# Optimization experiments

Measured on AMD Instinct MI355X. Metric: run time of the kernel, lower is better.

The kernel has to match this reference:

```python
import jax, jax.numpy as jnp
import numpy as np

N = 131072
F_IN = 256
FEATURES = 64
N_SOURCES = 32


def setup_inputs() -> dict:
    key = jax.random.key(0)
    k1, k2, k3 = jax.random.split(key, 3)
    x = jax.random.normal(k1, (N, F_IN), dtype=jnp.float32)
    source = jax.random.randint(k2, (N,), 0, N_SOURCES, dtype=jnp.int32)
    W = jax.random.normal(k3, (F_IN, N_SOURCES * FEATURES), dtype=jnp.float32) * (1.0 / np.sqrt(F_IN))
    b = jnp.zeros((N_SOURCES * FEATURES,), dtype=jnp.float32)
    return {"x": x, "source": source, "W": W, "b": b}


def reference(x, source, W, b):
    # Dense projection to all sources: (N, n_sources*features)
    y = jnp.dot(x, W) + b
    # Per-row gather of the slice belonging to this row's source id.
    # Equivalent to y[i, source[i]*FEATURES : (source[i]+1)*FEATURES].
    y = y.reshape(x.shape[0], N_SOURCES, FEATURES)
    out = jnp.take_along_axis(y, source[:, None, None].astype(jnp.int32), axis=1)
    return out[:, 0, :]  # (N, FEATURES)
```

## Files before the change

kernel.cpp:

```cpp
#include <hip/hip_runtime.h>

#define N_ROWS   131072
#define F_IN     256
#define FEAT     64
#define NSRC     32
#define WSTRIDE  (NSRC * FEAT)
#define NCH      32
#define CHUNK    4096
#define NCB      (N_ROWS / 256)
#define CBPC     16
#define CAPC     44
#define SEG      (CAPC + 1)
#define LCAP     320
#define TR       16
#define TPAD     66

#define MCHUNK   4096
#define LCAP1    512
#define KPAD     264

typedef __attribute__((ext_vector_type(8))) short  bf16x8;
typedef __attribute__((ext_vector_type(4))) float  f32x4;

#define WAITV(N)  asm volatile("s_waitcnt vmcnt(" #N ")" ::: "memory")
#define WAITLGKM() asm volatile("s_waitcnt lgkmcnt(0)" ::: "memory")
#define SBAR()    do { __builtin_amdgcn_s_barrier(); __builtin_amdgcn_sched_barrier(0); } while (0)

__device__ __forceinline__ unsigned short f2bf(float f) {
    union { float f; unsigned u; } c; c.f = f;
    unsigned r = c.u + 0x7fffu + ((c.u >> 16) & 1u);
    return (unsigned short)(r >> 16);
}

__device__ __forceinline__ bf16x8 pack8(f32x4 f0, f32x4 f1) {
    bf16x8 a;
    a[0] = (short)f2bf(f0[0]); a[1] = (short)f2bf(f0[1]);
    a[2] = (short)f2bf(f0[2]); a[3] = (short)f2bf(f0[3]);
    a[4] = (short)f2bf(f1[0]); a[5] = (short)f2bf(f1[1]);
    a[6] = (short)f2bf(f1[2]); a[7] = (short)f2bf(f1[3]);
    return a;
}

__global__ __launch_bounds__(256)
void compact_kernel(const int* __restrict__ src, int* __restrict__ ws) {
    __shared__ int lcnt[NSRC];
    const int tid = threadIdx.x;
    if (tid < NSRC) lcnt[tid] = 0;
    __syncthreads();
    const int row = blockIdx.x * 256 + tid;
    const int s   = src[row];
    const int p   = atomicAdd(&lcnt[s], 1);
    if (p < CAPC)
        ws[blockIdx.x * (NSRC * SEG) + s * SEG + 1 + p] = row;
    __syncthreads();
    if (tid < NSRC)
        ws[blockIdx.x * (NSRC * SEG) + tid * SEG] = min(lcnt[tid], CAPC);
}

__device__ __forceinline__ void stage_tile(const float* __restrict__ x,
                                           const int* lst, int count, int tile,
                                           int w, int lane, float* Abuf) {
    #pragma unroll
    for (int i = 0; i < 4; ++i) {
        const int r  = w * 4 + i;
        const int gi = min(tile * TR + r, count - 1);
        const float* srcp = x + (size_t)lst[gi] * F_IN + ((lane ^ (r & 7)) << 2);
        __builtin_amdgcn_global_load_lds(
            (const __attribute__((address_space(1))) void*)srcp,
            (__attribute__((address_space(3))) void*)(Abuf + r * F_IN),
            16, 0, 0);
    }
}

__global__ __launch_bounds__(256, 4)
void gemm_kernel(const float* __restrict__ x, const float* __restrict__ W,
                 const float* __restrict__ b, const int* __restrict__ ws,
                 float* __restrict__ out) {
    __shared__ __align__(16) float A[2][TR][F_IN];
    __shared__ __align__(16) float T[TR * TPAD];
    __shared__ int lst[LCAP];
    __shared__ int soff[CBPC + 1];

    const int tid = threadIdx.x;
    const int s   = blockIdx.x;
    const int c   = blockIdx.y;

    if (tid == 0) {
        int acc2 = 0;
        #pragma unroll
        for (int jj = 0; jj < CBPC; ++jj) {
            soff[jj] = acc2;
            acc2 += ws[(size_t)(c * CBPC + jj) * (NSRC * SEG) + s * SEG];
        }
        soff[CBPC] = acc2;
    }
    __syncthreads();
    const int count = min(soff[CBPC], LCAP);
    if (count == 0) return;
    {
        const int jj = tid >> 4, i0 = tid & 15;
        const size_t base = (size_t)(c * CBPC + jj) * (NSRC * SEG) + s * SEG;
        const int cj = ws[base];
        for (int i = i0; i < cj; i += 16) {
            const int pos = soff[jj] + i;
            if (pos < LCAP) lst[pos] = ws[base + 1 + i];
        }
    }
    __syncthreads();

    const int lane = tid & 63, w = tid >> 6;
    const int col  = lane & 15, quad = lane >> 4;

    const int ntiles = (count + TR - 1) / TR;

    stage_tile(x, lst, count, 0, w, lane, &A[0][0][0]);

    bf16x8 bb[8];
    {
        const float* wp = W + (size_t)(quad * 8) * WSTRIDE + s * FEAT + w * 16 + col;
        #pragma unroll
        for (int kk = 0; kk < 8; ++kk) {
            float tv[8];
            #pragma unroll
            for (int j = 0; j < 8; ++j)
                tv[j] = wp[(size_t)(kk * 32 + j) * WSTRIDE];
            bf16x8 v;
            #pragma unroll
            for (int j = 0; j < 8; ++j) v[j] = (short)f2bf(tv[j]);
            bb[kk] = v;
        }
    }
    const float bias = b[s * FEAT + w * 16 + col];

    for (int t = 0; t < ntiles; ++t) {
        if (t) WAITV(4); else WAITV(0);
        SBAR();
        if (t + 1 < ntiles)
            stage_tile(x, lst, count, t + 1, w, lane, &A[(t + 1) & 1][0][0]);

        f32x4 acc = (f32x4){0.f, 0.f, 0.f, 0.f};
        {
            const int key = col & 7;
            const float* arow = &A[t & 1][0][0] + col * F_IN;
            #pragma unroll
            for (int kk = 0; kk < 8; ++kk) {
                const int s0 = kk * 8 + quad * 2;
                const f32x4 lo = *(const f32x4*)(arow + (((s0    ) ^ key) << 2));
                const f32x4 hi = *(const f32x4*)(arow + (((s0 + 1) ^ key) << 2));
                unsigned u0, u1, u2, u3;
                asm("v_cvt_pk_bf16_f32 %0, %1, %2" : "=v"(u0) : "v"(lo[0]), "v"(lo[1]));
                asm("v_cvt_pk_bf16_f32 %0, %1, %2" : "=v"(u1) : "v"(lo[2]), "v"(lo[3]));
                asm("v_cvt_pk_bf16_f32 %0, %1, %2" : "=v"(u2) : "v"(hi[0]), "v"(hi[1]));
                asm("v_cvt_pk_bf16_f32 %0, %1, %2" : "=v"(u3) : "v"(hi[2]), "v"(hi[3]));
                union { unsigned u[4]; bf16x8 v; } cv;
                cv.u[0] = u0; cv.u[1] = u1; cv.u[2] = u2; cv.u[3] = u3;
                acc = __builtin_amdgcn_mfma_f32_16x16x32_bf16(cv.v, bb[kk], acc, 0, 0, 0);
            }
        }

        #pragma unroll
        for (int reg = 0; reg < 4; ++reg)
            T[(quad * 4 + reg) * TPAD + w * 16 + col] = acc[reg] + bias;
        WAITLGKM();
        SBAR();
        #pragma unroll
        for (int r = 0; r < 4; ++r) {
            const int gi = t * TR + w * 4 + r;
            if (gi < count)
                out[(size_t)lst[gi] * FEAT + lane] = T[(w * 4 + r) * TPAD + lane];
        }
    }
}

__global__ __launch_bounds__(256, 4)
void mono_kernel(const float* __restrict__ x, const int* __restrict__ src,
                 const float* __restrict__ W, const float* __restrict__ b,
                 float* __restrict__ out) {
    __shared__ __align__(16) unsigned short Wt[FEAT * KPAD];
    __shared__ int lst[LCAP1];
    __shared__ int cnt;
    const int tid = threadIdx.x, s = blockIdx.y, chunk0 = blockIdx.x * MCHUNK;
    if (tid == 0) cnt = 0;
    __syncthreads();
    {
        const int n = tid & 63, kp = (tid >> 6) * 2;
        #pragma unroll
        for (int k0 = 0; k0 < F_IN; k0 += 8) {
            const int k = k0 + kp;
            const float w0 = W[(size_t)k * WSTRIDE + s * FEAT + n];
            const float w1 = W[(size_t)(k + 1) * WSTRIDE + s * FEAT + n];
            *(unsigned*)&Wt[n * KPAD + k] = (unsigned)f2bf(w0) | ((unsigned)f2bf(w1) << 16);
        }
    }
    #pragma unroll
    for (int r = 0; r < MCHUNK / 256; ++r) {
        const int row = chunk0 + r * 256 + tid;
        if (src[row] == s) {
            const int p = atomicAdd(&cnt, 1);
            if (p < LCAP1) lst[p] = row;
        }
    }
    __syncthreads();
    const int count = cnt;
    if (count == 0) return;
    const int lane = tid & 63, w = tid >> 6, col = lane & 15, quad = lane >> 4;
    float bias[4];
    #pragma unroll
    for (int nt = 0; nt < 4; ++nt) bias[nt] = b[s * FEAT + nt * 16 + col];
    const int npass = (count + 63) >> 6;
    for (int pp = 0; pp < npass; ++pp) {
        const int base = pp * 64 + w * 16;
        const int ia = lst[min(base + col, count - 1)];
        const float* ap = x + (size_t)ia * F_IN + quad * 8;
        f32x4 av[16];
        #pragma unroll
        for (int kk = 0; kk < 8; ++kk) {
            av[2 * kk]     = *(const f32x4*)(ap + kk * 32);
            av[2 * kk + 1] = *(const f32x4*)(ap + kk * 32 + 4);
        }
        f32x4 acc[4];
        #pragma unroll
        for (int nt = 0; nt < 4; ++nt) acc[nt] = (f32x4){0.f, 0.f, 0.f, 0.f};
        #pragma unroll
        for (int kk = 0; kk < 8; ++kk) {
            const bf16x8 a = pack8(av[2 * kk], av[2 * kk + 1]);
            #pragma unroll
            for (int nt = 0; nt < 4; ++nt) {
                const bf16x8 bbv = *(const bf16x8*)&Wt[(nt * 16 + col) * KPAD + kk * 32 + quad * 8];
                acc[nt] = __builtin_amdgcn_mfma_f32_16x16x32_bf16(a, bbv, acc[nt], 0, 0, 0);
            }
        }
        #pragma unroll
        for (int reg = 0; reg < 4; ++reg) {
            const int gm = base + quad * 4 + reg;
            if (gm < count) {
                const int row = lst[gm];
                float* op = out + (size_t)row * FEAT;
                #pragma unroll
                for (int nt = 0; nt < 4; ++nt)
                    op[nt * 16 + col] = acc[nt][reg] + bias[nt];
            }
        }
    }
}

extern "C" void kernel_launch(void* const* d_in, const int* in_sizes, int n_in,
                              void* d_out, int out_size, void* d_ws, size_t ws_size,
                              hipStream_t stream) {
    const float* x   = (const float*)d_in[0];
    const int*   src = (const int*)d_in[1];
    const float* W   = (const float*)d_in[2];
    const float* b   = (const float*)d_in[3];
    float*       out = (float*)d_out;

    const size_t ws_needed = (size_t)NCB * NSRC * SEG * sizeof(int);
    if (ws_size >= ws_needed) {
        int* ws = (int*)d_ws;
        compact_kernel<<<dim3(NCB), dim3(256), 0, stream>>>(src, ws);
        gemm_kernel<<<dim3(NSRC, NCH), dim3(256), 0, stream>>>(x, W, b, ws, out);
    } else {
        mono_kernel<<<dim3(N_ROWS / MCHUNK, NSRC), dim3(256), 0, stream>>>(x, src, W, b, out);
    }
}
```

Baseline: 222.4 us.

## Pre-pack W to bf16 fragment layout in a separate kernel

Adds a pack_w kernel that converts W once per call into bf16 MFMA-fragment order in the workspace. Each gemm block then reads its B fragments with coalesced 16-byte loads instead of 64 strided fp32 loads and converts per block. The per-segment counts are also read in parallel into shared memory rather than serially by one thread. The cost is an extra kernel launch and a larger workspace requirement. If the workspace is too small, the launcher falls back to mono_kernel.

```diff
diff --git a/kernel.cpp b/kernel.cpp
--- a/kernel.cpp
+++ b/kernel.cpp
@@ -14,6 +14,8 @@
 #define LCAP     320
 #define TR       16
 #define TPAD     66
+#define WTOFF    (NCB * NSRC * SEG)
+#define WTINTS   (NSRC * FEAT * F_IN / 2)
 
 #define MCHUNK   4096
 #define LCAP1    512
@@ -39,6 +41,20 @@
     a[4] = (short)f2bf(f1[0]); a[5] = (short)f2bf(f1[1]);
     a[6] = (short)f2bf(f1[2]); a[7] = (short)f2bf(f1[3]);
     return a;
+}
+
+__global__ __launch_bounds__(256)
+void pack_w(const float* __restrict__ W, int* __restrict__ ws) {
+    const int idx  = blockIdx.x * 256 + threadIdx.x;
+    const int lane = idx & 63, kk = (idx >> 6) & 7, w = (idx >> 9) & 3, s = idx >> 11;
+    const int col  = lane & 15, quad = lane >> 4;
+    const int n    = s * FEAT + w * 16 + col;
+    const int k0   = kk * 32 + quad * 8;
+    bf16x8 v;
+    #pragma unroll
+    for (int j = 0; j < 8; ++j)
+        v[j] = (short)f2bf(W[(size_t)(k0 + j) * WSTRIDE + n]);
+    ((bf16x8*)(ws + WTOFF))[idx] = v;
 }
 
 __global__ __launch_bounds__(256)
@@ -73,26 +89,26 @@
 }
 
 __global__ __launch_bounds__(256, 4)
-void gemm_kernel(const float* __restrict__ x, const float* __restrict__ W,
-                 const float* __restrict__ b, const int* __restrict__ ws,
-                 float* __restrict__ out) {
+void gemm_kernel(const float* __restrict__ x, const float* __restrict__ b,
+                 const int* __restrict__ ws, float* __restrict__ out) {
     __shared__ __align__(16) float A[2][TR][F_IN];
     __shared__ __align__(16) float T[TR * TPAD];
     __shared__ int lst[LCAP];
+    __shared__ int scnt[CBPC];
     __shared__ int soff[CBPC + 1];
 
     const int tid = threadIdx.x;
     const int s   = blockIdx.x;
     const int c   = blockIdx.y;
 
+    if (tid < CBPC)
+        scnt[tid] = ws[(size_t)(c * CBPC + tid) * (NSRC * SEG) + s * SEG];
+    __syncthreads();
     if (tid == 0) {
-        int acc2 = 0;
-        #pragma unroll
-        for (int jj = 0; jj < CBPC; ++jj) {
-            soff[jj] = acc2;
-            acc2 += ws[(size_t)(c * CBPC + jj) * (NSRC * SEG) + s * SEG];
-        }
-        soff[CBPC] = acc2;
+        int a = 0;
+        #pragma unroll
+        for (int jj = 0; jj < CBPC; ++jj) { soff[jj] = a; a += scnt[jj]; }
+        soff[CBPC] = a;
     }
     __syncthreads();
     const int count = min(soff[CBPC], LCAP);
@@ -100,7 +116,7 @@
     {
         const int jj = tid >> 4, i0 = tid & 15;
         const size_t base = (size_t)(c * CBPC + jj) * (NSRC * SEG) + s * SEG;
-        const int cj = ws[base];
+        const int cj = scnt[jj];
         for (int i = i0; i < cj; i += 16) {
             const int pos = soff[jj] + i;
             if (pos < LCAP) lst[pos] = ws[base + 1 + i];
@@ -117,18 +133,9 @@
 
     bf16x8 bb[8];
     {
-        const float* wp = W + (size_t)(quad * 8) * WSTRIDE + s * FEAT + w * 16 + col;
-        #pragma unroll
-        for (int kk = 0; kk < 8; ++kk) {
-            float tv[8];
-            #pragma unroll
-            for (int j = 0; j < 8; ++j)
-                tv[j] = wp[(size_t)(kk * 32 + j) * WSTRIDE];
-            bf16x8 v;
-            #pragma unroll
-            for (int j = 0; j < 8; ++j) v[j] = (short)f2bf(tv[j]);
-            bb[kk] = v;
-        }
+        const bf16x8* wp = (const bf16x8*)(ws + WTOFF) + ((s * 4 + w) * 8) * 64 + lane;
+        #pragma unroll
+        for (int kk = 0; kk < 8; ++kk) bb[kk] = wp[kk * 64];
     }
     const float bias = b[s * FEAT + w * 16 + col];
 
@@ -253,11 +260,12 @@
     const float* b   = (const float*)d_in[3];
     float*       out = (float*)d_out;
 
-    const size_t ws_needed = (size_t)NCB * NSRC * SEG * sizeof(int);
+    const size_t ws_needed = (size_t)(WTOFF + WTINTS) * sizeof(int);
     if (ws_size >= ws_needed) {
         int* ws = (int*)d_ws;
+        pack_w<<<dim3(256), dim3(256), 0, stream>>>(W, ws);
         compact_kernel<<<dim3(NCB), dim3(256), 0, stream>>>(src, ws);
-        gemm_kernel<<<dim3(NSRC, NCH), dim3(256), 0, stream>>>(x, W, b, ws, out);
+        gemm_kernel<<<dim3(NSRC, NCH), dim3(256), 0, stream>>>(x, b, ws, out);
     } else {
         mono_kernel<<<dim3(N_ROWS / MCHUNK, NSRC), dim3(256), 0, stream>>>(x, src, W, b, out);
     }
```

Result: faster. 217.1 us (-2.4%).
